# Kernel optimization log

Hardware: AMD Instinct MI355X
Metric: run time of the kernel (lower is better)

Reference implementation:

```python
import jax, jax.numpy as jnp
import numpy as np

B, S, DIN, DOUT = 4, 4096, 4096, 4096
W_SCALE = 0.02  # kaiming-ish scale; keeps values inside fp8 range


def setup_inputs() -> dict:
    key = jax.random.key(0)
    k1, k2, k3 = jax.random.split(key, 3)
    x = jax.random.normal(k1, (B, S, DIN), dtype=jnp.float16)
    weight = (jax.random.normal(k2, (DOUT, DIN), dtype=jnp.float32) * W_SCALE).astype(jnp.float16)
    bias = (jax.random.normal(k3, (DOUT,), dtype=jnp.float32) * W_SCALE).astype(jnp.float16)
    return {"x": x, "weight": weight, "bias": bias}


def reference(x, weight, bias):
    # Emulate torch._scaled_mm: activations quantized to fp8 e5m2,
    # weight (transposed) quantized to fp8 e4m3fn, scale_a = scale_b = 1.0,
    # accumulate in fp32, add fp16 bias, output fp16.
    out_shape = x.shape[:-1] + (weight.shape[0],)
    x8 = x.reshape(-1, x.shape[-1]).astype(jnp.float8_e5m2)       # [M, DIN]
    w8 = weight.T.astype(jnp.float8_e4m3fn)                        # [DIN, DOUT]
    scale = jnp.float32(1.0)  # scale_a * scale_b
    acc = jnp.matmul(x8.astype(jnp.float32), w8.astype(jnp.float32))  # [M, DOUT] fp32 accum
    out = (acc * scale + bias.astype(jnp.float32)).astype(jnp.float16)
    return out.reshape(out_shape)
```

## Files before the change

kernel.cpp:

```cpp
#include <hip/hip_runtime.h>
#include <hip/hip_fp16.h>

#define M_DIM 16384
#define N_DIM 4096
#define K_DIM 4096

typedef __attribute__((ext_vector_type(16))) float f32x16;
typedef __attribute__((ext_vector_type(4)))  int   i32x4;
typedef __attribute__((ext_vector_type(8)))  int   i32x8;

template<bool E4M3>
__global__ __launch_bounds__(256) void quant_tile_kernel(
    const float* __restrict__ in,
    uint4* __restrict__ out,
    int ngrp)
{
  int t = blockIdx.x * 256 + threadIdx.x;
  if (t >= ngrp) return;
  const int g    = t & 1023;
  const int tile = t >> 10;
  const int kt   = tile & 63;
  const int bt   = tile >> 6;
  const int sb   = g >> 7;
  const int half = (g >> 6) & 1;
  const int l    = g & 63;
  const int row  = bt * 256 + sb * 32 + (l & 31);
  const int k    = kt * 64 + (l >> 5) * 32 + half * 16;

  const float4* p = reinterpret_cast<const float4*>(in + (size_t)row * K_DIM + k);
  float4 v0 = p[0], v1 = p[1], v2 = p[2], v3 = p[3];
  int w0 = 0, w1 = 0, w2 = 0, w3 = 0;
  if (E4M3) {
    w0 = __builtin_amdgcn_cvt_pk_fp8_f32(v0.x, v0.y, w0, false);
    w0 = __builtin_amdgcn_cvt_pk_fp8_f32(v0.z, v0.w, w0, true);
    w1 = __builtin_amdgcn_cvt_pk_fp8_f32(v1.x, v1.y, w1, false);
    w1 = __builtin_amdgcn_cvt_pk_fp8_f32(v1.z, v1.w, w1, true);
    w2 = __builtin_amdgcn_cvt_pk_fp8_f32(v2.x, v2.y, w2, false);
    w2 = __builtin_amdgcn_cvt_pk_fp8_f32(v2.z, v2.w, w2, true);
    w3 = __builtin_amdgcn_cvt_pk_fp8_f32(v3.x, v3.y, w3, false);
    w3 = __builtin_amdgcn_cvt_pk_fp8_f32(v3.z, v3.w, w3, true);
  } else {
    w0 = __builtin_amdgcn_cvt_pk_bf8_f32(v0.x, v0.y, w0, false);
    w0 = __builtin_amdgcn_cvt_pk_bf8_f32(v0.z, v0.w, w0, true);
    w1 = __builtin_amdgcn_cvt_pk_bf8_f32(v1.x, v1.y, w1, false);
    w1 = __builtin_amdgcn_cvt_pk_bf8_f32(v1.z, v1.w, w1, true);
    w2 = __builtin_amdgcn_cvt_pk_bf8_f32(v2.x, v2.y, w2, false);
    w2 = __builtin_amdgcn_cvt_pk_bf8_f32(v2.z, v2.w, w2, true);
    w3 = __builtin_amdgcn_cvt_pk_bf8_f32(v3.x, v3.y, w3, false);
    w3 = __builtin_amdgcn_cvt_pk_bf8_f32(v3.z, v3.w, w3, true);
  }
  out[t] = make_uint4((unsigned)w0, (unsigned)w1, (unsigned)w2, (unsigned)w3);
}

__global__ __launch_bounds__(256, 1) void gemm_fp8_kernel(
    const unsigned char* __restrict__ Aq,
    const unsigned char* __restrict__ Wq,
    const float* __restrict__ bias,
    float* __restrict__ C)
{
  __shared__ __align__(16) unsigned char lds[65536];

  const int tid  = threadIdx.x;
  const int lane = tid & 63;
  const int wave = tid >> 6;
  const int wr   = wave >> 1;
  const int wc   = wave & 1;

  const int bid = blockIdx.x;
  const int swz = (bid & 7) * 128 + (bid >> 3);
  const int bni = swz >> 6;
  const int bmi = swz & 63;

  const unsigned char* tA = Aq + (size_t)bmi * (64 * 16384);
  const unsigned char* tB = Wq + (size_t)bni * (64 * 16384);

  const size_t t16 = (size_t)tid * 16;
  const int    w1k = wave * 1024;

#define STAGE(gb, lo_)                                                      \
  __builtin_amdgcn_global_load_lds(                                        \
      (const __attribute__((address_space(1))) void*)((gb) + t16),          \
      (__attribute__((address_space(3))) void*)(lds + (lo_) + w1k), 16, 0, 0)

#define STAGE_TILE(tp, ldsbase)                                             \
  STAGE(tA + (tp),         (ldsbase) + 0);                                  \
  STAGE(tA + (tp) + 4096,  (ldsbase) + 4096);                               \
  STAGE(tA + (tp) + 8192,  (ldsbase) + 8192);                               \
  STAGE(tA + (tp) + 12288, (ldsbase) + 12288);                              \
  STAGE(tB + (tp),         (ldsbase) + 16384);                              \
  STAGE(tB + (tp) + 4096,  (ldsbase) + 20480);                              \
  STAGE(tB + (tp) + 8192,  (ldsbase) + 24576);                              \
  STAGE(tB + (tp) + 12288, (ldsbase) + 28672)

#define RD8(dst, off)                                                       \
  { const unsigned char* _p = lds + (off) + lane * 16;                      \
    union { i32x8 v; i32x4 h[2]; } _u;                                      \
    _u.h[0] = *(const i32x4*)_p;                                            \
    _u.h[1] = *(const i32x4*)(_p + 1024);                                   \
    (dst) = _u.v; }

#define MFMA(d, a, b)                                                       \
  d = __builtin_amdgcn_mfma_scale_f32_32x32x64_f8f6f4(                      \
      a, b, d, 1 , 0 , 0, 0x7F7F7F7F, 0, 0x7F7F7F7F)

#define SB __builtin_amdgcn_sched_barrier(0)

  const int aoff = wr * 8192;
  const int boff = 16384 + wc * 8192;

  f32x16 acc[4][4] = {};

  STAGE_TILE(0, 0);
  SB;
  STAGE_TILE(16384, 32768);
  SB;
  asm volatile("s_waitcnt vmcnt(8)" ::: "memory");
  SB;
  __builtin_amdgcn_s_barrier();

  for (int kt = 0; kt < 64; ++kt) {
    const int bufo = (kt & 1) * 32768;
    const size_t tp = (size_t)((kt + 2) & 63) * 16384;

    i32x8 b0, b1, b2, b3, a0, a1, a2, a3;
    RD8(b0, bufo + boff + 0 * 2048);
    RD8(b1, bufo + boff + 1 * 2048);
    RD8(b2, bufo + boff + 2 * 2048);
    RD8(b3, bufo + boff + 3 * 2048);
    RD8(a0, bufo + aoff + 0 * 2048);
    RD8(a1, bufo + aoff + 1 * 2048);
    RD8(a2, bufo + aoff + 2 * 2048);
    RD8(a3, bufo + aoff + 3 * 2048);
    SB;
    asm volatile("s_waitcnt lgkmcnt(6)" ::: "memory");
    SB;
    MFMA(acc[0][0], a0, b0); MFMA(acc[0][1], a0, b1);
    MFMA(acc[0][2], a0, b2); MFMA(acc[0][3], a0, b3);
    SB;
    asm volatile("s_waitcnt lgkmcnt(4)" ::: "memory");
    SB;
    MFMA(acc[1][0], a1, b0); MFMA(acc[1][1], a1, b1);
    MFMA(acc[1][2], a1, b2); MFMA(acc[1][3], a1, b3);
    SB;
    asm volatile("s_waitcnt lgkmcnt(2)" ::: "memory");
    SB;
    MFMA(acc[2][0], a2, b0); MFMA(acc[2][1], a2, b1);
    MFMA(acc[2][2], a2, b2); MFMA(acc[2][3], a2, b3);
    SB;
    asm volatile("s_waitcnt lgkmcnt(0)" ::: "memory");
    SB;
    MFMA(acc[3][0], a3, b0); MFMA(acc[3][1], a3, b1);
    MFMA(acc[3][2], a3, b2); MFMA(acc[3][3], a3, b3);
    SB;
    __builtin_amdgcn_s_barrier();
    STAGE_TILE(tp, bufo);
    SB;
    asm volatile("s_waitcnt vmcnt(8)" ::: "memory");
    SB;
    __builtin_amdgcn_s_barrier();
  }
#undef STAGE
#undef STAGE_TILE
#undef RD8
#undef MFMA
#undef SB

  #pragma unroll
  for (int n = 0; n < 4; ++n) {
    const int col = bni * 256 + wc * 128 + n * 32 + (lane & 31);
    const float bv = bias[col];
    #pragma unroll
    for (int m = 0; m < 4; ++m) {
      const int rbase = bmi * 256 + wr * 128 + m * 32 + ((lane >> 5) << 2);
      #pragma unroll
      for (int r = 0; r < 16; ++r) {
        const int row = rbase + (r & 3) + 8 * (r >> 2);
        C[(size_t)row * N_DIM + col] =
            __half2float(__float2half_rn(acc[m][n][r] + bv));
      }
    }
  }
}

extern "C" void kernel_launch(void* const* d_in, const int* in_sizes, int n_in,
                              void* d_out, int out_size, void* d_ws, size_t ws_size,
                              hipStream_t stream) {
  const float* x  = (const float*)d_in[0];
  const float* w  = (const float*)d_in[1];
  const float* bs = (const float*)d_in[2];
  float* out = (float*)d_out;

  unsigned char* xq = (unsigned char*)d_ws;
  unsigned char* wq = (unsigned char*)d_ws + (size_t)M_DIM * K_DIM;

  const int ngx = (M_DIM * K_DIM) / 16;
  const int ngw = (N_DIM * K_DIM) / 16;
  quant_tile_kernel<false><<<ngx / 256, 256, 0, stream>>>(x, (uint4*)xq, ngx);
  quant_tile_kernel<true ><<<ngw / 256, 256, 0, stream>>>(w, (uint4*)wq, ngw);

  gemm_fp8_kernel<<<1024, 256, 0, stream>>>(xq, wq, bs, out);
}
```

Baseline: 409.7 us.

## Move FP8 GEMM to 8 waves with triple-buffered LDS and interleaved staging

Doubles the GEMM block from 4 to 8 waves, each owning a 128x64 output sub-tile, and grows LDS from double to triple buffering (96KB). Global-to-LDS loads for tile t+2 are split into four chunks, each issued between the per-row MFMA groups. Barriers and s_setprio raise MFMA priority so loads overlap with compute. It also changes the block-to-tile swizzle ordering. The cost is more barriers per k-tile and a larger LDS footprint that limits residency to one block per CU.

```diff
diff --git a/kernel.cpp b/kernel.cpp
--- a/kernel.cpp
+++ b/kernel.cpp
@@ -52,24 +52,24 @@
   out[t] = make_uint4((unsigned)w0, (unsigned)w1, (unsigned)w2, (unsigned)w3);
 }
 
-__global__ __launch_bounds__(256, 1) void gemm_fp8_kernel(
+__global__ __launch_bounds__(512, 2) void gemm_fp8_kernel(
     const unsigned char* __restrict__ Aq,
     const unsigned char* __restrict__ Wq,
     const float* __restrict__ bias,
     float* __restrict__ C)
 {
-  __shared__ __align__(16) unsigned char lds[65536];
+  __shared__ __align__(16) unsigned char lds[98304];
 
   const int tid  = threadIdx.x;
   const int lane = tid & 63;
   const int wave = tid >> 6;
-  const int wr   = wave >> 1;
-  const int wc   = wave & 1;
+  const int wr   = wave >> 2;
+  const int wc   = wave & 3;
 
   const int bid = blockIdx.x;
   const int swz = (bid & 7) * 128 + (bid >> 3);
-  const int bni = swz >> 6;
-  const int bmi = swz & 63;
+  const int bmi = swz >> 4;
+  const int bni = swz & 15;
 
   const unsigned char* tA = Aq + (size_t)bmi * (64 * 16384);
   const unsigned char* tB = Wq + (size_t)bni * (64 * 16384);
@@ -81,16 +81,6 @@
   __builtin_amdgcn_global_load_lds(                                        \
       (const __attribute__((address_space(1))) void*)((gb) + t16),          \
       (__attribute__((address_space(3))) void*)(lds + (lo_) + w1k), 16, 0, 0)
-
-#define STAGE_TILE(tp, ldsbase)                                             \
-  STAGE(tA + (tp),         (ldsbase) + 0);                                  \
-  STAGE(tA + (tp) + 4096,  (ldsbase) + 4096);                               \
-  STAGE(tA + (tp) + 8192,  (ldsbase) + 8192);                               \
-  STAGE(tA + (tp) + 12288, (ldsbase) + 12288);                              \
-  STAGE(tB + (tp),         (ldsbase) + 16384);                              \
-  STAGE(tB + (tp) + 4096,  (ldsbase) + 20480);                              \
-  STAGE(tB + (tp) + 8192,  (ldsbase) + 24576);                              \
-  STAGE(tB + (tp) + 12288, (ldsbase) + 28672)
 
 #define RD8(dst, off)                                                       \
   { const unsigned char* _p = lds + (off) + lane * 16;                      \
@@ -103,71 +93,99 @@
   d = __builtin_amdgcn_mfma_scale_f32_32x32x64_f8f6f4(                      \
       a, b, d, 1 , 0 , 0, 0x7F7F7F7F, 0, 0x7F7F7F7F)
 
-#define SB __builtin_amdgcn_sched_barrier(0)
+#define SBAR __builtin_amdgcn_sched_barrier(0)
+#define BAR  __builtin_amdgcn_s_barrier()
+#define DSW  asm volatile("s_waitcnt lgkmcnt(0)" ::: "memory"); SBAR
+#define VMW4 asm volatile("s_waitcnt vmcnt(4)" ::: "memory"); SBAR
+#define P1   __builtin_amdgcn_s_setprio(1)
+#define P0   __builtin_amdgcn_s_setprio(0)
 
   const int aoff = wr * 8192;
-  const int boff = 16384 + wc * 8192;
-
-  f32x16 acc[4][4] = {};
-
-  STAGE_TILE(0, 0);
-  SB;
-  STAGE_TILE(16384, 32768);
-  SB;
-  asm volatile("s_waitcnt vmcnt(8)" ::: "memory");
-  SB;
-  __builtin_amdgcn_s_barrier();
-
-  for (int kt = 0; kt < 64; ++kt) {
-    const int bufo = (kt & 1) * 32768;
-    const size_t tp = (size_t)((kt + 2) & 63) * 16384;
-
-    i32x8 b0, b1, b2, b3, a0, a1, a2, a3;
-    RD8(b0, bufo + boff + 0 * 2048);
-    RD8(b1, bufo + boff + 1 * 2048);
-    RD8(b2, bufo + boff + 2 * 2048);
-    RD8(b3, bufo + boff + 3 * 2048);
-    RD8(a0, bufo + aoff + 0 * 2048);
-    RD8(a1, bufo + aoff + 1 * 2048);
-    RD8(a2, bufo + aoff + 2 * 2048);
-    RD8(a3, bufo + aoff + 3 * 2048);
-    SB;
-    asm volatile("s_waitcnt lgkmcnt(6)" ::: "memory");
-    SB;
-    MFMA(acc[0][0], a0, b0); MFMA(acc[0][1], a0, b1);
-    MFMA(acc[0][2], a0, b2); MFMA(acc[0][3], a0, b3);
-    SB;
-    asm volatile("s_waitcnt lgkmcnt(4)" ::: "memory");
-    SB;
-    MFMA(acc[1][0], a1, b0); MFMA(acc[1][1], a1, b1);
-    MFMA(acc[1][2], a1, b2); MFMA(acc[1][3], a1, b3);
-    SB;
-    asm volatile("s_waitcnt lgkmcnt(2)" ::: "memory");
-    SB;
-    MFMA(acc[2][0], a2, b0); MFMA(acc[2][1], a2, b1);
-    MFMA(acc[2][2], a2, b2); MFMA(acc[2][3], a2, b3);
-    SB;
-    asm volatile("s_waitcnt lgkmcnt(0)" ::: "memory");
-    SB;
-    MFMA(acc[3][0], a3, b0); MFMA(acc[3][1], a3, b1);
-    MFMA(acc[3][2], a3, b2); MFMA(acc[3][3], a3, b3);
-    SB;
-    __builtin_amdgcn_s_barrier();
-    STAGE_TILE(tp, bufo);
-    SB;
-    asm volatile("s_waitcnt vmcnt(8)" ::: "memory");
-    SB;
-    __builtin_amdgcn_s_barrier();
+  const int boff = 16384 + wc * 4096;
+
+  f32x16 acc[4][2] = {};
+  i32x8 aU, aV, bE0, bE1, bO0, bO1;
+
+  STAGE(tA,         0);      STAGE(tA + 8192,  8192);
+  STAGE(tB,         16384);  STAGE(tB + 8192,  24576);
+  SBAR;
+  STAGE(tA + 16384, 32768);  STAGE(tA + 24576, 40960);
+  STAGE(tB + 16384, 49152);  STAGE(tB + 24576, 57344);
+  SBAR;
+  VMW4;
+  BAR;
+
+  int cA = 0, cB = 32768, cC = 65536;
+
+  for (int it = 0; it < 32; ++it) {
+    const int t = it << 1;
+    const size_t tpC = (size_t)((t + 2) & 63) * 16384;
+    const size_t tpD = (size_t)((t + 3) & 63) * 16384;
+
+    RD8(bE0, cA + boff);  RD8(bE1, cA + boff + 2048);
+    RD8(aU,  cA + aoff);
+    STAGE(tA + tpC, cC);
+    BAR; DSW; P1;
+    MFMA(acc[0][0], aU, bE0); MFMA(acc[0][1], aU, bE1);
+    P0; BAR;
+    RD8(aV, cA + aoff + 2048);
+    STAGE(tA + tpC + 8192, cC + 8192);
+    BAR; DSW; P1;
+    MFMA(acc[1][0], aV, bE0); MFMA(acc[1][1], aV, bE1);
+    P0; BAR;
+    RD8(aU, cA + aoff + 4096);
+    STAGE(tB + tpC, cC + 16384);
+    BAR; DSW; P1;
+    MFMA(acc[2][0], aU, bE0); MFMA(acc[2][1], aU, bE1);
+    P0; BAR;
+    RD8(aV, cA + aoff + 6144);
+    STAGE(tB + tpC + 8192, cC + 24576);
+    BAR; DSW; P1;
+    MFMA(acc[3][0], aV, bE0); MFMA(acc[3][1], aV, bE1);
+    P0;
+    VMW4;
+    BAR;
+
+    RD8(bO0, cB + boff);  RD8(bO1, cB + boff + 2048);
+    RD8(aU,  cB + aoff);
+    STAGE(tA + tpD, cA);
+    BAR; DSW; P1;
+    MFMA(acc[0][0], aU, bO0); MFMA(acc[0][1], aU, bO1);
+    P0; BAR;
+    RD8(aV, cB + aoff + 2048);
+    STAGE(tA + tpD + 8192, cA + 8192);
+    BAR; DSW; P1;
+    MFMA(acc[1][0], aV, bO0); MFMA(acc[1][1], aV, bO1);
+    P0; BAR;
+    RD8(aU, cB + aoff + 4096);
+    STAGE(tB + tpD, cA + 16384);
+    BAR; DSW; P1;
+    MFMA(acc[2][0], aU, bO0); MFMA(acc[2][1], aU, bO1);
+    P0; BAR;
+    RD8(aV, cB + aoff + 6144);
+    STAGE(tB + tpD + 8192, cA + 24576);
+    BAR; DSW; P1;
+    MFMA(acc[3][0], aV, bO0); MFMA(acc[3][1], aV, bO1);
+    P0;
+    VMW4;
+    BAR;
+
+    const int nA = cC, nB = cA, nC = cB;
+    cA = nA; cB = nB; cC = nC;
   }
 #undef STAGE
-#undef STAGE_TILE
 #undef RD8
 #undef MFMA
-#undef SB
+#undef SBAR
+#undef BAR
+#undef DSW
+#undef VMW4
+#undef P1
+#undef P0
 
   #pragma unroll
-  for (int n = 0; n < 4; ++n) {
-    const int col = bni * 256 + wc * 128 + n * 32 + (lane & 31);
+  for (int n = 0; n < 2; ++n) {
+    const int col = bni * 256 + wc * 64 + n * 32 + (lane & 31);
     const float bv = bias[col];
     #pragma unroll
     for (int m = 0; m < 4; ++m) {
@@ -198,5 +216,5 @@
   quant_tile_kernel<false><<<ngx / 256, 256, 0, stream>>>(x, (uint4*)xq, ngx);
   quant_tile_kernel<true ><<<ngw / 256, 256, 0, stream>>>(w, (uint4*)wq, ngw);
 
-  gemm_fp8_kernel<<<1024, 256, 0, stream>>>(xq, wq, bs, out);
+  gemm_fp8_kernel<<<1024, 512, 0, stream>>>(xq, wq, bs, out);
 }
```

After: 353.7 us. 13.7% less time.
